# Optimization experiments

Measured on AMD Instinct MI355X. Metric: run time of the kernel, lower is better.

Reference implementation:

```python
import jax, jax.numpy as jnp
import numpy as np

B, N, C, L, O = 32, 16000, 128, 512, 35
FS = 16000
F_LO, F_HI = 100.0, 8000.0
BETA = 0.9        # Leaky decay (snntorch Leaky beta)
AN_UTH = 0.5      # auditory-nerve threshold (an_uth)
TH = 1.0          # default threshold for later stages
STELI_STD = (1.0, 2.0, 3.0)


def _gammatone_kernels():
    # 4th-order gammatone impulse responses, ERB-spaced center freqs.
    erb = lambda f: 21.4 * np.log10(4.37 * f / 1000.0 + 1.0)
    erb_inv = lambda e: (10 ** (e / 21.4) - 1.0) * 1000.0 / 4.37
    cfs = erb_inv(np.linspace(erb(F_LO), erb(F_HI), C))          # [C]
    t = np.arange(L) / FS                                        # [L]
    bw = 1.019 * 24.7 * (4.37 * cfs / 1000.0 + 1.0)              # [C]
    g = (t[None, :] ** 3) * np.exp(-2 * np.pi * bw[:, None] * t[None, :]) \
        * np.cos(2 * np.pi * cfs[:, None] * t[None, :])          # [C,L]
    g = g / np.maximum(np.linalg.norm(g, axis=1, keepdims=True), 1e-12)
    return jnp.asarray(g, dtype=jnp.float32)


def _gauss_w(std, n):
    # fixed Gaussian lateral connectivity (OSF / stellate layer)
    i = np.arange(n, dtype=np.float64)
    w = np.exp(-((i[:, None] - i[None, :]) ** 2) / (2.0 * std ** 2))
    w = w / w.sum(axis=1, keepdims=True)
    return jnp.asarray(w, dtype=jnp.float32)


@jax.custom_vjp
def spike(x):
    return (x > 0).astype(x.dtype)

def _spk_fwd(x):
    return spike(x), x

def _spk_bwd(x, g):
    # ATan-style surrogate gradient (snntorch default)
    return (g / (1.0 + (jnp.pi * x) ** 2),)

spike.defvjp(_spk_fwd, _spk_bwd)


def setup_inputs() -> dict:
    key = jax.random.key(0)
    ks = jax.random.split(key, 8)
    s = 1.0 / np.sqrt(C)
    return {
        "audio": jax.random.normal(ks[0], (B, N), jnp.float32),
        "gt_kernels": _gammatone_kernels(),
        "W_an": jax.random.normal(ks[1], (C, C), jnp.float32) * s,
        "b_an": jnp.zeros((C,), jnp.float32),
        "W_b": _gauss_w(STELI_STD[0], C),
        "W_m": _gauss_w(STELI_STD[1], C),
        "W_n": _gauss_w(STELI_STD[2], C),
        "W_ic": jax.random.normal(ks[2], (C, C), jnp.float32) * s,
        "b_ic": jnp.zeros((C,), jnp.float32),
        "W_ac": jax.random.normal(ks[3], (O, C), jnp.float32) * s,
        "b_ac": jnp.zeros((O,), jnp.float32),
        "ihc_win": 160,
    }


def reference(audio, gt_kernels, W_an, b_an, W_b, W_m, W_n, W_ic, b_ic, W_ac, b_ac, ihc_win):
    # Cochlea: gammatone FIR filterbank.  [B,N] -> [B,C,N]
    x = jax.lax.conv_general_dilated(
        audio[:, None, :], gt_kernels[:, None, :], (1,), "SAME",
        dimension_numbers=("NCH", "OIH", "NCH"))
    # Inner hair cell: half-wave rectify + windowed average (envelope, downsample)
    x = jax.nn.relu(x)
    T = N // ihc_win
    x = x[..., : T * ihc_win].reshape(B, C, T, ihc_win).mean(-1)   # [B,C,T]
    x = x.transpose(2, 0, 1)                                       # [T,B,C]

    def leaky(mem, cur, th):
        mem = BETA * mem + cur
        spk = spike(mem - th)
        return spk, mem - spk * th   # reset by subtraction

    def step(carry, xt):
        m_an, m_b, m_m, m_n, m_ic, m_ac = carry
        s_an, m_an = leaky(m_an, xt @ W_an.T + b_an, AN_UTH)
        s_b,  m_b  = leaky(m_b,  s_an @ W_b.T, TH)
        s_m,  m_m  = leaky(m_m,  s_b @ W_m.T, TH)
        s_n,  m_n  = leaky(m_n,  s_m @ W_n.T, TH)
        s_ic, m_ic = leaky(m_ic, s_n @ W_ic.T + b_ic, TH)
        s_ac, m_ac = leaky(m_ac, s_ic @ W_ac.T + b_ac, TH)
        return (m_an, m_b, m_m, m_n, m_ic, m_ac), (s_ac, m_ac)

    z = jnp.zeros((B, C), x.dtype)
    za = jnp.zeros((B, O), x.dtype)
    _, (spk_rec, mem_rec) = jax.lax.scan(step, (z, z, z, z, z, za), x)
    # [T,B,O] -> [B,T,O]; stack (spk, mem) like the torch module's tuple output
    return jnp.stack([spk_rec.transpose(1, 0, 2), mem_rec.transpose(1, 0, 2)])
```

## Files before the change

### kernel.cpp

```cpp
#include <hip/hip_runtime.h>
#include <math.h>

#define BB 32
#define NN 16000
#define CC 128
#define LL 512
#define OO 35
#define TT 100
#define BTO (BB * TT * OO)
#define FSR 16000.0

#define SEG 320
#define NSEG 50
#define SPAN 833

#define WT_OFF   0
#define PAR_OFF  0x100000
#define CUR_OFF  0
#define XT_OFF   0x350000

__global__ __launch_bounds__(512) void gt_tables(double* __restrict__ Wt,
                                                 double* __restrict__ par) {
    const int c = blockIdx.x;
    const int l = threadIdx.x;
    const double TWO_PI = 6.283185307179586476925287;
    const double e_lo = 21.4 * log10(4.37 * 100.0 / 1000.0 + 1.0);
    const double e_hi = 21.4 * log10(4.37 * 8000.0 / 1000.0 + 1.0);
    const double step = (e_hi - e_lo) / 127.0;
    const double e = (c == 127) ? e_hi : e_lo + c * step;
    const double cf = (pow(10.0, e / 21.4) - 1.0) * 1000.0 / 4.37;
    const double bw = 1.019 * 24.7 * (4.37 * cf / 1000.0 + 1.0);

    const double t = (double)l / FSR;
    const double env = exp(-TWO_PI * bw * t);
    const double ang = TWO_PI * cf * t;
    const double wr = env * cos(ang);
    const double wi = env * sin(ang);
    Wt[(l * CC + c) * 2 + 0] = wr;
    Wt[(l * CC + c) * 2 + 1] = wi;

    __shared__ double red[512];
    const double l3 = (double)l * (double)l * (double)l;
    const double q = l3 * wr;
    red[l] = q * q;
    __syncthreads();
    for (int s = 256; s > 0; s >>= 1) {
        if (l < s) red[l] += red[l + s];
        __syncthreads();
    }
    if (l == 0) {
        double* p = par + c * 16;
        const double a1 = TWO_PI * bw / FSR, th1 = TWO_PI * cf / FSR;
        const double e1 = exp(-a1);
        p[0] = e1 * cos(th1);
        p[1] = e1 * sin(th1);
        const double aL = TWO_PI * bw * (512.0 / FSR), thL = TWO_PI * cf * (512.0 / FSR);
        const double eL = exp(-aL);
        const double pr = eL * cos(thL), pim = eL * sin(thL);
        p[2] = pr;              p[3] = pim;
        p[4] = 512.0 * pr;      p[5] = 512.0 * pim;
        p[6] = 130816.0 * pr;   p[7] = 130816.0 * pim;
        p[8] = 22238720.0 * pr; p[9] = 22238720.0 * pim;
        p[10] = 1.0 / sqrt(red[0]);
    }
}

#define CONV_STEP(AIN, AOUT)                                              \
    {                                                                     \
        const double ain = (AIN), aout = (AOUT);                          \
        const double t3r = d3r + d2r, t3i = d3i + d2i;                    \
        const double t2r = d2r + d1r, t2i = d2i + d1i;                    \
        const double t1r = d1r + d0r, t1i = d1i + d0i;                    \
        d3r = fma(t3r, rr, fma(t3i, -ri, -cr3 * aout));                   \
        d3i = fma(t3r, ri, fma(t3i,  rr, -ci3 * aout));                   \
        d2r = fma(t2r, rr, fma(t2i, -ri, -cr2 * aout));                   \
        d2i = fma(t2r, ri, fma(t2i,  rr, -ci2 * aout));                   \
        d1r = fma(t1r, rr, fma(t1i, -ri, -cr1 * aout));                   \
        d1i = fma(t1r, ri, fma(t1i,  rr, -ci1 * aout));                   \
        const double o0r = fma(d0r, rr, fma(d0i, -ri, fma(-cr0, aout, ain))); \
        const double o0i = fma(d0r, ri, fma(d0i,  rr, -ci0 * aout));      \
        d0r = o0r; d0i = o0i;                                             \
        const double yv = scale * fma(6.0, d2r + d3r, d1r);               \
        float yf = (float)yv;                                             \
        yf = yf > 0.0f ? yf : 0.0f;                                       \
        wsum += (double)yf;                                               \
        if (++cnt == 160) {                                               \
            xt[widx] = (float)(wsum / 160.0);                             \
            widx -= CC;                                                   \
            wsum = 0.0;                                                   \
            cnt = 0;                                                      \
        }                                                                 \
    }

#define WARM_TAP(W, AV)                                                   \
    {                                                                     \
        const double av = (AV);                                           \
        d0r = fma((W).x, av, d0r);           d0i = fma((W).y, av, d0i);   \
        const double t1 = av * b1;                                        \
        d1r = fma((W).x, t1, d1r);           d1i = fma((W).y, t1, d1i);   \
        const double t2 = av * b2;                                        \
        d2r = fma((W).x, t2, d2r);           d2i = fma((W).y, t2, d2i);   \
        const double t3 = av * b3;                                        \
        d3r = fma((W).x, t3, d3r);           d3i = fma((W).y, t3, d3i);   \
        b3 += b2; b2 += b1; b1 += 1.0;                                    \
    }

__global__ __launch_bounds__(64, 4) void conv_rec(
    const float* __restrict__ audio,
    const double* __restrict__ Wt,
    const double* __restrict__ par,
    float* __restrict__ xt)
{
    const int blk = blockIdx.x;
    const int half = blk & 1;
    const int segblk = blk >> 1;
    const int b = segblk / NSEG;
    const int seg = segblk % NSEG;
    const int n0 = seg * SEG;
    const int c = half * 64 + threadIdx.x;

    __shared__ __align__(16) double aldsD[SPAN + 3];
    for (int i = threadIdx.x; i < SPAN; i += 64) {
        const int g = n0 - 256 + i;
        aldsD[1 + i] = (g >= 0 && g < NN) ? (double)audio[b * NN + g] : 0.0;
    }
    __syncthreads();

    const double* p = par + c * 16;
    const double rr = p[0], ri = p[1];
    const double cr0 = p[2], ci0 = p[3], cr1 = p[4], ci1 = p[5];
    const double cr2 = p[6], ci2 = p[7], cr3 = p[8], ci3 = p[9];
    const double scale = p[10];

    double d0r = 0, d0i = 0, d1r = 0, d1i = 0, d2r = 0, d2i = 0, d3r = 0, d3i = 0;
    double b1 = 0.0, b2 = 0.0, b3 = 0.0;

    const double2* wp = reinterpret_cast<const double2*>(&Wt[c * 2]);
    double2 w0 = wp[0 * CC], w1 = wp[1 * CC], w2 = wp[2 * CC], w3 = wp[3 * CC];
    double2 a01 = *reinterpret_cast<const double2*>(&aldsD[SEG + 2]);
    double2 a23 = *reinterpret_cast<const double2*>(&aldsD[SEG + 4]);

    for (int l = 0; l < 512; l += 4) {
        const int lp = (l + 4) & 511;
        double2 nw0 = wp[(lp + 0) * CC];
        double2 nw1 = wp[(lp + 1) * CC];
        double2 nw2 = wp[(lp + 2) * CC];
        double2 nw3 = wp[(lp + 3) * CC];
        double2 na01 = *reinterpret_cast<const double2*>(&aldsD[SEG + 2 + lp]);
        double2 na23 = *reinterpret_cast<const double2*>(&aldsD[SEG + 4 + lp]);
        WARM_TAP(w0, a01.x);
        WARM_TAP(w1, a01.y);
        WARM_TAP(w2, a23.x);
        WARM_TAP(w3, a23.y);
        w0 = nw0; w1 = nw1; w2 = nw2; w3 = nw3; a01 = na01; a23 = na23;
    }

    double wsum = 0.0;
    int widx = (b * TT + seg * (SEG / 160) + (SEG / 160 - 1)) * CC + c;
    int cnt = 0;

    double2 ain2  = *reinterpret_cast<const double2*>(&aldsD[SEG]);
    double2 aout2 = *reinterpret_cast<const double2*>(&aldsD[SEG + 512]);
    #pragma unroll 2
    for (int m = 0; m < SEG; m += 2) {
        const int mp = (m + 2 < SEG) ? m + 2 : 0;
        double2 nain  = *reinterpret_cast<const double2*>(&aldsD[SEG - mp]);
        double2 naout = *reinterpret_cast<const double2*>(&aldsD[SEG + 512 - mp]);
        CONV_STEP(ain2.y, aout2.y);
        CONV_STEP(ain2.x, aout2.x);
        ain2 = nain; aout2 = naout;
    }
}

__global__ __launch_bounds__(128) void an_cur_kernel(
    const float* __restrict__ xt, const float* __restrict__ W_an,
    const float* __restrict__ b_an, double* __restrict__ cur_d)
{
    __shared__ float xr[CC];
    const int row = blockIdx.x;
    const int c = threadIdx.x;
    xr[c] = xt[row * CC + c];
    __syncthreads();
    const float* wr = W_an + c * CC;
    double acc = (double)b_an[c];
    #pragma unroll
    for (int k = 0; k < CC; k += 4) {
        float4 w4 = *reinterpret_cast<const float4*>(wr + k);
        acc += (double)w4.x * (double)xr[k]
             + (double)w4.y * (double)xr[k+1]
             + (double)w4.z * (double)xr[k+2]
             + (double)w4.w * (double)xr[k+3];
    }
    cur_d[row * CC + c] = acc;
}

#define R1 8
#define W1 17
#define R2 16
#define W2 33
#define R3 24
#define W3 49
#define SPW 24

__global__ __launch_bounds__(512, 1) void snn_kernel(
    const double* __restrict__ cur_an,
    const float* __restrict__ W_b, const float* __restrict__ W_m, const float* __restrict__ W_n,
    const float* __restrict__ W_ic, const float* __restrict__ b_ic,
    const float* __restrict__ W_ac, const float* __restrict__ b_ac,
    float* __restrict__ out)
{
    __shared__ __align__(16) double sa[2][176], sb[2][176], sm[2][176];
    __shared__ __align__(16) double sn_[2][CC];
    __shared__ __align__(16) double icp[2][4][CC];
    __shared__ __align__(16) double sic[2][CC];
    __shared__ double acp[2][2][36];
    __shared__ __align__(16) double wacd[OO][132];

    const int b = blockIdx.x;
    const int tid = threadIdx.x;
    const int wid = tid >> 6;
    const int l = tid & 63;
    const int c0 = 2 * l, c1 = 2 * l + 1;

    {
        double* z0 = &sa[0][0]; double* z1 = &sb[0][0]; double* z2 = &sm[0][0];
        for (int i = tid; i < 352; i += 512) { z0[i] = 0.0; z1[i] = 0.0; z2[i] = 0.0; }
    }
    for (int i = tid; i < OO * CC; i += 512)
        wacd[i >> 7][i & 127] = (double)W_ac[i];

    float wband[2 * W3];
    double bic0 = 0.0, bic1 = 0.0, bacv = 0.0;
    double mm0 = 0.0, mm1 = 0.0;
    double mic0 = 0.0, mic1 = 0.0;
    double macv = 0.0;
    double2 pf0 = make_double2(0.0, 0.0), pf1 = make_double2(0.0, 0.0);

    if (wid == 0) {
        pf0 = *reinterpret_cast<const double2*>(&cur_an[(b * TT + 0) * CC + c0]);
        pf1 = *reinterpret_cast<const double2*>(&cur_an[(b * TT + 1) * CC + c0]);
        bic0 = (double)b_ic[c0]; bic1 = (double)b_ic[c1];
        if (l < OO) bacv = (double)b_ac[l];
    } else if (wid == 1) {
        #pragma unroll
        for (int x = 0; x < W1; ++x) {
            int k0 = c0 - R1 + x, k1 = c1 - R1 + x;
            wband[x]      = (k0 >= 0 && k0 < CC) ? W_b[c0 * CC + k0] : 0.f;
            wband[W1 + x] = (k1 >= 0 && k1 < CC) ? W_b[c1 * CC + k1] : 0.f;
        }
    } else if (wid == 2) {
        #pragma unroll
        for (int x = 0; x < W2; ++x) {
            int k0 = c0 - R2 + x, k1 = c1 - R2 + x;
            wband[x]      = (k0 >= 0 && k0 < CC) ? W_m[c0 * CC + k0] : 0.f;
            wband[W2 + x] = (k1 >= 0 && k1 < CC) ? W_m[c1 * CC + k1] : 0.f;
        }
    } else if (wid == 3) {
        #pragma unroll
        for (int x = 0; x < W3; ++x) {
            int k0 = c0 - R3 + x, k1 = c1 - R3 + x;
            wband[x]      = (k0 >= 0 && k0 < CC) ? W_n[c0 * CC + k0] : 0.f;
            wband[W3 + x] = (k1 >= 0 && k1 < CC) ? W_n[c1 * CC + k1] : 0.f;
        }
    } else {
        const int q = wid - 4;
        #pragma unroll
        for (int j = 0; j < 32; ++j) {
            wband[j]      = W_ic[c0 * CC + 32 * q + j];
            wband[32 + j] = W_ic[c1 * CC + 32 * q + j];
        }
    }
    __syncthreads();

    for (int tick = 0; tick < TT + 7; ++tick) {
        if (wid == 0) {
            if (tick < TT) {
                double2 cv = pf0; pf0 = pf1;
                if (tick + 2 < TT)
                    pf1 = *reinterpret_cast<const double2*>(&cur_an[(b * TT + tick + 2) * CC + c0]);
                double me0 = 0.9 * mm0 + cv.x; double d0 = me0 - 0.5;
                bool s0 = d0 > 0.0; mm0 = s0 ? d0 : me0;
                double me1 = 0.9 * mm1 + cv.y; double d1 = me1 - 0.5;
                bool s1 = d1 > 0.0; mm1 = s1 ? d1 : me1;
                *reinterpret_cast<double2*>(&sa[tick & 1][SPW + c0]) =
                    make_double2(s0 ? 1.0 : 0.0, s1 ? 1.0 : 0.0);
            }
            const int t5 = tick - 5;
            if (t5 >= 0 && t5 < TT) {
                const int p = t5 & 1;
                double2 q0 = *reinterpret_cast<const double2*>(&icp[p][0][c0]);
                double2 q1 = *reinterpret_cast<const double2*>(&icp[p][1][c0]);
                double2 q2 = *reinterpret_cast<const double2*>(&icp[p][2][c0]);
                double2 q3 = *reinterpret_cast<const double2*>(&icp[p][3][c0]);
                double acc0 = ((q0.x + q1.x) + (q2.x + q3.x)) + bic0;
                double acc1 = ((q0.y + q1.y) + (q2.y + q3.y)) + bic1;
                double mem0 = 0.9 * mic0 + acc0; double dd0 = mem0 - 1.0;
                bool s0 = dd0 > 0.0; mic0 = s0 ? dd0 : mem0;
                double mem1 = 0.9 * mic1 + acc1; double dd1 = mem1 - 1.0;
                bool s1 = dd1 > 0.0; mic1 = s1 ? dd1 : mem1;
                *reinterpret_cast<double2*>(&sic[p][c0]) =
                    make_double2(s0 ? 1.0 : 0.0, s1 ? 1.0 : 0.0);
            }
            const int t6 = tick - 6;
            if (l < 6 && t6 >= 0 && t6 < TT) {
                const int p = t6 & 1, r = 32 + (l >> 1), h = l & 1;
                const double* sp = &sic[p][h * 64];
                const double* wr = &wacd[r][h * 64];
                double a0 = 0, a1 = 0, a2 = 0, a3 = 0;
                #pragma unroll
                for (int k = 0; k < 64; k += 4) {
                    double2 v01 = *reinterpret_cast<const double2*>(&sp[k]);
                    double2 v23 = *reinterpret_cast<const double2*>(&sp[k + 2]);
                    double2 w01 = *reinterpret_cast<const double2*>(&wr[k]);
                    double2 w23 = *reinterpret_cast<const double2*>(&wr[k + 2]);
                    a0 = fma(w01.x, v01.x, a0);
                    a1 = fma(w01.y, v01.y, a1);
                    a2 = fma(w23.x, v23.x, a2);
                    a3 = fma(w23.y, v23.y, a3);
                }
                acp[p][h][r] = (a0 + a1) + (a2 + a3);
            }
            const int t7 = tick - 7;
            if (l < OO && t7 >= 0 && t7 < TT) {
                const int p = t7 & 1;
                double acc = (acp[p][0][l] + acp[p][1][l]) + bacv;
                double mem = 0.9 * macv + acc;
                double d = mem - 1.0; bool s = d > 0.0;
                macv = s ? d : mem;
                const int idx = (b * TT + t7) * OO + l;
                out[idx] = s ? 1.f : 0.f;
                out[BTO + idx] = (float)macv;
            }
        } else if (wid == 1) {
            const int t = tick - 1;
            if (t >= 0 && t < TT) {
                const int p = t & 1;
                const double2* pw = reinterpret_cast<const double2*>(&sa[p][SPW + c0 - R1]);
                double aA0 = 0, aA1 = 0, aB0 = 0, aB1 = 0;
                #pragma unroll
                for (int i = 0; i < 9; ++i) {
                    double2 v = pw[i];
                    double vx = v.x, vy = v.y;
                    if (2 * i < W1)     aA0 = fma((double)wband[2 * i],          vx, aA0);
                    if (2 * i + 1 < W1) aA1 = fma((double)wband[2 * i + 1],      vy, aA1);
                    if (2 * i >= 1)     aB0 = fma((double)wband[W1 + 2 * i - 1], vx, aB0);
                    if (2 * i < W1)     aB1 = fma((double)wband[W1 + 2 * i],     vy, aB1);
                }
                double me0 = 0.9 * mm0 + (aA0 + aA1); double d0 = me0 - 1.0;
                bool s0 = d0 > 0.0; mm0 = s0 ? d0 : me0;
                double me1 = 0.9 * mm1 + (aB0 + aB1); double d1 = me1 - 1.0;
                bool s1 = d1 > 0.0; mm1 = s1 ? d1 : me1;
                *reinterpret_cast<double2*>(&sb[p][SPW + c0]) =
                    make_double2(s0 ? 1.0 : 0.0, s1 ? 1.0 : 0.0);
            }
            const int t6 = tick - 6;
            if (t6 >= 0 && t6 < TT) {
                const int p = t6 & 1, r = l >> 1, h = l & 1;
                const double* sp = &sic[p][h * 64];
                const double* wr = &wacd[r][h * 64];
                double a0 = 0, a1 = 0, a2 = 0, a3 = 0;
                #pragma unroll
                for (int k = 0; k < 64; k += 4) {
                    double2 v01 = *reinterpret_cast<const double2*>(&sp[k]);
                    double2 v23 = *reinterpret_cast<const double2*>(&sp[k + 2]);
                    double2 w01 = *reinterpret_cast<const double2*>(&wr[k]);
                    double2 w23 = *reinterpret_cast<const double2*>(&wr[k + 2]);
                    a0 = fma(w01.x, v01.x, a0);
                    a1 = fma(w01.y, v01.y, a1);
                    a2 = fma(w23.x, v23.x, a2);
                    a3 = fma(w23.y, v23.y, a3);
                }
                acp[p][h][r] = (a0 + a1) + (a2 + a3);
            }
        } else if (wid == 2) {
            const int t = tick - 2;
            if (t >= 0 && t < TT) {
                const int p = t & 1;
                const double2* pw = reinterpret_cast<const double2*>(&sb[p][SPW + c0 - R2]);
                double aA0 = 0, aA1 = 0, aB0 = 0, aB1 = 0;
                #pragma unroll
                for (int i = 0; i < 17; ++i) {
                    double2 v = pw[i];
                    double vx = v.x, vy = v.y;
                    if (2 * i < W2)     aA0 = fma((double)wband[2 * i],          vx, aA0);
                    if (2 * i + 1 < W2) aA1 = fma((double)wband[2 * i + 1],      vy, aA1);
                    if (2 * i >= 1)     aB0 = fma((double)wband[W2 + 2 * i - 1], vx, aB0);
                    if (2 * i < W2)     aB1 = fma((double)wband[W2 + 2 * i],     vy, aB1);
                }
                double me0 = 0.9 * mm0 + (aA0 + aA1); double d0 = me0 - 1.0;
                bool s0 = d0 > 0.0; mm0 = s0 ? d0 : me0;
                double me1 = 0.9 * mm1 + (aB0 + aB1); double d1 = me1 - 1.0;
                bool s1 = d1 > 0.0; mm1 = s1 ? d1 : me1;
                *reinterpret_cast<double2*>(&sm[p][SPW + c0]) =
                    make_double2(s0 ? 1.0 : 0.0, s1 ? 1.0 : 0.0);
            }
        } else if (wid == 3) {
            const int t = tick - 3;
            if (t >= 0 && t < TT) {
                const int p = t & 1;
                const double2* pw = reinterpret_cast<const double2*>(&sm[p][SPW + c0 - R3]);
                double aA0 = 0, aA1 = 0, aB0 = 0, aB1 = 0;
                #pragma unroll
                for (int i = 0; i < 25; ++i) {
                    double2 v = pw[i];
                    double vx = v.x, vy = v.y;
                    if (2 * i < W3)     aA0 = fma((double)wband[2 * i],          vx, aA0);
                    if (2 * i + 1 < W3) aA1 = fma((double)wband[2 * i + 1],      vy, aA1);
                    if (2 * i >= 1)     aB0 = fma((double)wband[W3 + 2 * i - 1], vx, aB0);
                    if (2 * i < W3)     aB1 = fma((double)wband[W3 + 2 * i],     vy, aB1);
                }
                double me0 = 0.9 * mm0 + (aA0 + aA1); double d0 = me0 - 1.0;
                bool s0 = d0 > 0.0; mm0 = s0 ? d0 : me0;
                double me1 = 0.9 * mm1 + (aB0 + aB1); double d1 = me1 - 1.0;
                bool s1 = d1 > 0.0; mm1 = s1 ? d1 : me1;
                *reinterpret_cast<double2*>(&sn_[p][c0]) =
                    make_double2(s0 ? 1.0 : 0.0, s1 ? 1.0 : 0.0);
            }
        } else {
            const int t = tick - 4;
            if (t >= 0 && t < TT) {
                const int p = t & 1, q = wid - 4;
                const double* sp = &sn_[p][32 * q];
                double a0 = 0, a1 = 0, g0 = 0, g1 = 0;
                #pragma unroll
                for (int k = 0; k < 32; k += 4) {
                    double2 va = *reinterpret_cast<const double2*>(&sp[k]);
                    double2 vb = *reinterpret_cast<const double2*>(&sp[k + 2]);
                    a0 = fma((double)wband[k],          va.x, a0);
                    a1 = fma((double)wband[k + 1],      va.y, a1);
                    a0 = fma((double)wband[k + 2],      vb.x, a0);
                    a1 = fma((double)wband[k + 3],      vb.y, a1);
                    g0 = fma((double)wband[32 + k],     va.x, g0);
                    g1 = fma((double)wband[32 + k + 1], va.y, g1);
                    g0 = fma((double)wband[32 + k + 2], vb.x, g0);
                    g1 = fma((double)wband[32 + k + 3], vb.y, g1);
                }
                *reinterpret_cast<double2*>(&icp[p][q][c0]) =
                    make_double2(a0 + a1, g0 + g1);
            }
        }
        __syncthreads();
    }
}

extern "C" void kernel_launch(void* const* d_in, const int* in_sizes, int n_in,
                              void* d_out, int out_size, void* d_ws, size_t ws_size,
                              hipStream_t stream) {
    const float* audio = (const float*)d_in[0];
    const float* W_an  = (const float*)d_in[2];
    const float* b_an  = (const float*)d_in[3];
    const float* W_b   = (const float*)d_in[4];
    const float* W_m   = (const float*)d_in[5];
    const float* W_n   = (const float*)d_in[6];
    const float* W_ic  = (const float*)d_in[7];
    const float* b_ic  = (const float*)d_in[8];
    const float* W_ac  = (const float*)d_in[9];
    const float* b_ac  = (const float*)d_in[10];

    char* ws = (char*)d_ws;
    double* Wt    = (double*)(ws + WT_OFF);
    double* par   = (double*)(ws + PAR_OFF);
    double* cur_d = (double*)(ws + CUR_OFF);
    float*  xt    = (float*)(ws + XT_OFF);
    float*  out   = (float*)d_out;

    gt_tables<<<dim3(CC), dim3(512), 0, stream>>>(Wt, par);
    conv_rec<<<dim3(BB * NSEG * 2), dim3(64), 0, stream>>>(audio, Wt, par, xt);
    an_cur_kernel<<<dim3(BB * TT), dim3(128), 0, stream>>>(xt, W_an, b_an, cur_d);
    snn_kernel<<<dim3(BB), dim3(512), 0, stream>>>(
        cur_d, W_b, W_m, W_n, W_ic, b_ic, W_ac, b_ac, out);
}
```

Measured before the change: 321.3 us.

## Process two channels per thread and double segment length in gammatone recursion

Each conv_rec thread now runs the recursive gammatone filter for two channels (c and c+64), and each block covers a 640-sample segment instead of 320. The warm-up pass over the 512-tap kernel is shared across both channels, and longer segments cut the number of warm-ups per output sample, which was a large share of the FP64 work. The cost is fewer blocks (800 instead of 3200 single-wave blocks), more registers per thread (launch bounds relaxed to 1), and a longer serial recursion per thread, which can lower occupancy and latency hiding on a latency-bound FP64 dependency chain.

After: 432.3 us. 34.6% more time.

```diff
diff --git a/kernel.cpp b/kernel.cpp
--- a/kernel.cpp
+++ b/kernel.cpp
@@ -10,9 +10,9 @@
 #define BTO (BB * TT * OO)
 #define FSR 16000.0
 
-#define SEG 320
-#define NSEG 50
-#define SPAN 833
+#define SEG 640
+#define NSEG 25
+#define SPAN 1153
 
 #define WT_OFF   0
 #define PAR_OFF  0x100000
@@ -65,59 +65,68 @@
     }
 }
 
-#define CONV_STEP(AIN, AOUT)                                              \
+#define CH_STEP(S)                                                        \
+    {                                                                     \
+        const double t3r = d3r##S + d2r##S, t3i = d3i##S + d2i##S;        \
+        const double t2r = d2r##S + d1r##S, t2i = d2i##S + d1i##S;        \
+        const double t1r = d1r##S + d0r##S, t1i = d1i##S + d0i##S;        \
+        d3r##S = fma(t3r, rr##S, fma(t3i, -ri##S, -cr3##S * aout));       \
+        d3i##S = fma(t3r, ri##S, fma(t3i,  rr##S, -ci3##S * aout));       \
+        d2r##S = fma(t2r, rr##S, fma(t2i, -ri##S, -cr2##S * aout));       \
+        d2i##S = fma(t2r, ri##S, fma(t2i,  rr##S, -ci2##S * aout));       \
+        d1r##S = fma(t1r, rr##S, fma(t1i, -ri##S, -cr1##S * aout));       \
+        d1i##S = fma(t1r, ri##S, fma(t1i,  rr##S, -ci1##S * aout));       \
+        const double o0r = fma(d0r##S, rr##S, fma(d0i##S, -ri##S, fma(-cr0##S, aout, ain))); \
+        const double o0i = fma(d0r##S, ri##S, fma(d0i##S,  rr##S, -ci0##S * aout)); \
+        d0r##S = o0r; d0i##S = o0i;                                       \
+        const double yv = scale##S * fma(6.0, d2r##S + d3r##S, d1r##S);   \
+        float yf = (float)yv;                                             \
+        yf = yf > 0.0f ? yf : 0.0f;                                       \
+        wsum##S += (double)yf;                                            \
+    }
+
+#define CONV_STEP2(AIN, AOUT)                                             \
     {                                                                     \
         const double ain = (AIN), aout = (AOUT);                          \
-        const double t3r = d3r + d2r, t3i = d3i + d2i;                    \
-        const double t2r = d2r + d1r, t2i = d2i + d1i;                    \
-        const double t1r = d1r + d0r, t1i = d1i + d0i;                    \
-        d3r = fma(t3r, rr, fma(t3i, -ri, -cr3 * aout));                   \
-        d3i = fma(t3r, ri, fma(t3i,  rr, -ci3 * aout));                   \
-        d2r = fma(t2r, rr, fma(t2i, -ri, -cr2 * aout));                   \
-        d2i = fma(t2r, ri, fma(t2i,  rr, -ci2 * aout));                   \
-        d1r = fma(t1r, rr, fma(t1i, -ri, -cr1 * aout));                   \
-        d1i = fma(t1r, ri, fma(t1i,  rr, -ci1 * aout));                   \
-        const double o0r = fma(d0r, rr, fma(d0i, -ri, fma(-cr0, aout, ain))); \
-        const double o0i = fma(d0r, ri, fma(d0i,  rr, -ci0 * aout));      \
-        d0r = o0r; d0i = o0i;                                             \
-        const double yv = scale * fma(6.0, d2r + d3r, d1r);               \
-        float yf = (float)yv;                                             \
-        yf = yf > 0.0f ? yf : 0.0f;                                       \
-        wsum += (double)yf;                                               \
+        CH_STEP(A)                                                        \
+        CH_STEP(B)                                                        \
         if (++cnt == 160) {                                               \
-            xt[widx] = (float)(wsum / 160.0);                             \
+            xt[widx] = (float)(wsumA / 160.0);                            \
+            xt[widx + 64] = (float)(wsumB / 160.0);                       \
             widx -= CC;                                                   \
-            wsum = 0.0;                                                   \
+            wsumA = 0.0; wsumB = 0.0;                                     \
             cnt = 0;                                                      \
         }                                                                 \
     }
 
-#define WARM_TAP(W, AV)                                                   \
+#define WARM_TAP2(WA, WB, AV)                                             \
     {                                                                     \
         const double av = (AV);                                           \
-        d0r = fma((W).x, av, d0r);           d0i = fma((W).y, av, d0i);   \
         const double t1 = av * b1;                                        \
-        d1r = fma((W).x, t1, d1r);           d1i = fma((W).y, t1, d1i);   \
         const double t2 = av * b2;                                        \
-        d2r = fma((W).x, t2, d2r);           d2i = fma((W).y, t2, d2i);   \
         const double t3 = av * b3;                                        \
-        d3r = fma((W).x, t3, d3r);           d3i = fma((W).y, t3, d3i);   \
+        d0rA = fma((WA).x, av, d0rA);        d0iA = fma((WA).y, av, d0iA);\
+        d1rA = fma((WA).x, t1, d1rA);        d1iA = fma((WA).y, t1, d1iA);\
+        d2rA = fma((WA).x, t2, d2rA);        d2iA = fma((WA).y, t2, d2iA);\
+        d3rA = fma((WA).x, t3, d3rA);        d3iA = fma((WA).y, t3, d3iA);\
+        d0rB = fma((WB).x, av, d0rB);        d0iB = fma((WB).y, av, d0iB);\
+        d1rB = fma((WB).x, t1, d1rB);        d1iB = fma((WB).y, t1, d1iB);\
+        d2rB = fma((WB).x, t2, d2rB);        d2iB = fma((WB).y, t2, d2iB);\
+        d3rB = fma((WB).x, t3, d3rB);        d3iB = fma((WB).y, t3, d3iB);\
         b3 += b2; b2 += b1; b1 += 1.0;                                    \
     }
 
-__global__ __launch_bounds__(64, 4) void conv_rec(
+__global__ __launch_bounds__(64, 1) void conv_rec(
     const float* __restrict__ audio,
     const double* __restrict__ Wt,
     const double* __restrict__ par,
     float* __restrict__ xt)
 {
     const int blk = blockIdx.x;
-    const int half = blk & 1;
-    const int segblk = blk >> 1;
-    const int b = segblk / NSEG;
-    const int seg = segblk % NSEG;
+    const int b = blk / NSEG;
+    const int seg = blk % NSEG;
     const int n0 = seg * SEG;
-    const int c = half * 64 + threadIdx.x;
+    const int cA = threadIdx.x;
 
     __shared__ __align__(16) double aldsD[SPAN + 3];
     for (int i = threadIdx.x; i < SPAN; i += 64) {
@@ -126,48 +135,51 @@
     }
     __syncthreads();
 
-    const double* p = par + c * 16;
-    const double rr = p[0], ri = p[1];
-    const double cr0 = p[2], ci0 = p[3], cr1 = p[4], ci1 = p[5];
-    const double cr2 = p[6], ci2 = p[7], cr3 = p[8], ci3 = p[9];
-    const double scale = p[10];
-
-    double d0r = 0, d0i = 0, d1r = 0, d1i = 0, d2r = 0, d2i = 0, d3r = 0, d3i = 0;
+    const double* pA = par + cA * 16;
+    const double rrA = pA[0], riA = pA[1];
+    const double cr0A = pA[2], ci0A = pA[3], cr1A = pA[4], ci1A = pA[5];
+    const double cr2A = pA[6], ci2A = pA[7], cr3A = pA[8], ci3A = pA[9];
+    const double scaleA = pA[10];
+    const double* pB = par + (cA + 64) * 16;
+    const double rrB = pB[0], riB = pB[1];
+    const double cr0B = pB[2], ci0B = pB[3], cr1B = pB[4], ci1B = pB[5];
+    const double cr2B = pB[6], ci2B = pB[7], cr3B = pB[8], ci3B = pB[9];
+    const double scaleB = pB[10];
+
+    double d0rA = 0, d0iA = 0, d1rA = 0, d1iA = 0, d2rA = 0, d2iA = 0, d3rA = 0, d3iA = 0;
+    double d0rB = 0, d0iB = 0, d1rB = 0, d1iB = 0, d2rB = 0, d2iB = 0, d3rB = 0, d3iB = 0;
     double b1 = 0.0, b2 = 0.0, b3 = 0.0;
 
-    const double2* wp = reinterpret_cast<const double2*>(&Wt[c * 2]);
-    double2 w0 = wp[0 * CC], w1 = wp[1 * CC], w2 = wp[2 * CC], w3 = wp[3 * CC];
+    const double2* wpA = reinterpret_cast<const double2*>(&Wt[cA * 2]);
+    const double2* wpB = reinterpret_cast<const double2*>(&Wt[(cA + 64) * 2]);
+    double2 wA0 = wpA[0 * CC], wA1 = wpA[1 * CC];
+    double2 wB0 = wpB[0 * CC], wB1 = wpB[1 * CC];
     double2 a01 = *reinterpret_cast<const double2*>(&aldsD[SEG + 2]);
-    double2 a23 = *reinterpret_cast<const double2*>(&aldsD[SEG + 4]);
-
-    for (int l = 0; l < 512; l += 4) {
-        const int lp = (l + 4) & 511;
-        double2 nw0 = wp[(lp + 0) * CC];
-        double2 nw1 = wp[(lp + 1) * CC];
-        double2 nw2 = wp[(lp + 2) * CC];
-        double2 nw3 = wp[(lp + 3) * CC];
+
+    for (int l = 0; l < 512; l += 2) {
+        const int lp = (l + 2) & 511;
+        double2 nwA0 = wpA[(lp + 0) * CC];
+        double2 nwA1 = wpA[(lp + 1) * CC];
+        double2 nwB0 = wpB[(lp + 0) * CC];
+        double2 nwB1 = wpB[(lp + 1) * CC];
         double2 na01 = *reinterpret_cast<const double2*>(&aldsD[SEG + 2 + lp]);
-        double2 na23 = *reinterpret_cast<const double2*>(&aldsD[SEG + 4 + lp]);
-        WARM_TAP(w0, a01.x);
-        WARM_TAP(w1, a01.y);
-        WARM_TAP(w2, a23.x);
-        WARM_TAP(w3, a23.y);
-        w0 = nw0; w1 = nw1; w2 = nw2; w3 = nw3; a01 = na01; a23 = na23;
-    }
-
-    double wsum = 0.0;
-    int widx = (b * TT + seg * (SEG / 160) + (SEG / 160 - 1)) * CC + c;
+        WARM_TAP2(wA0, wB0, a01.x);
+        WARM_TAP2(wA1, wB1, a01.y);
+        wA0 = nwA0; wA1 = nwA1; wB0 = nwB0; wB1 = nwB1; a01 = na01;
+    }
+
+    double wsumA = 0.0, wsumB = 0.0;
+    int widx = (b * TT + seg * (SEG / 160) + (SEG / 160 - 1)) * CC + cA;
     int cnt = 0;
 
     double2 ain2  = *reinterpret_cast<const double2*>(&aldsD[SEG]);
     double2 aout2 = *reinterpret_cast<const double2*>(&aldsD[SEG + 512]);
-    #pragma unroll 2
     for (int m = 0; m < SEG; m += 2) {
         const int mp = (m + 2 < SEG) ? m + 2 : 0;
         double2 nain  = *reinterpret_cast<const double2*>(&aldsD[SEG - mp]);
         double2 naout = *reinterpret_cast<const double2*>(&aldsD[SEG + 512 - mp]);
-        CONV_STEP(ain2.y, aout2.y);
-        CONV_STEP(ain2.x, aout2.x);
+        CONV_STEP2(ain2.y, aout2.y);
+        CONV_STEP2(ain2.x, aout2.x);
         ain2 = nain; aout2 = naout;
     }
 }
@@ -465,7 +477,7 @@
     float*  out   = (float*)d_out;
 
     gt_tables<<<dim3(CC), dim3(512), 0, stream>>>(Wt, par);
-    conv_rec<<<dim3(BB * NSEG * 2), dim3(64), 0, stream>>>(audio, Wt, par, xt);
+    conv_rec<<<dim3(BB * NSEG), dim3(64), 0, stream>>>(audio, Wt, par, xt);
     an_cur_kernel<<<dim3(BB * TT), dim3(128), 0, stream>>>(xt, W_an, b_an, cur_d);
     snn_kernel<<<dim3(BB), dim3(512), 0, stream>>>(
         cur_d, W_b, W_m, W_n, W_ic, b_ic, W_ac, b_ac, out);
```
